# Kernel tuning notes

Hardware: AMD Instinct MI355X
Metric: run time of the kernel (lower is better)

Reference implementation:

```python
import jax, jax.numpy as jnp
import numpy as np

N_HEAD = 8
D_MODEL = 512
D_HEAD = D_MODEL // N_HEAD
D_HIDDEN = 2048
LN_EPS = 1e-5


def setup_inputs() -> dict:
    key = jax.random.key(0)
    ks = jax.random.split(key, 13)
    s = 0.02
    return {
        "spatial_features": jax.random.normal(ks[0], (4096, 64, D_MODEL), dtype=jnp.float32),
        "Wk": jax.random.normal(ks[1], (D_MODEL, D_MODEL), dtype=jnp.float32) * s,
        "bk": jnp.zeros((D_MODEL,), dtype=jnp.float32),
        "Wv": jax.random.normal(ks[2], (D_MODEL, D_MODEL), dtype=jnp.float32) * s,
        "bv": jnp.zeros((D_MODEL,), dtype=jnp.float32),
        "score_w": jax.random.normal(ks[3], (N_HEAD, D_HEAD), dtype=jnp.float32) * s,
        "score_b": jnp.zeros((N_HEAD,), dtype=jnp.float32),
        "W1": jax.random.normal(ks[4], (D_MODEL, D_HIDDEN), dtype=jnp.float32) * s,
        "b1": jnp.zeros((D_HIDDEN,), dtype=jnp.float32),
        "W2": jax.random.normal(ks[5], (D_HIDDEN, D_MODEL), dtype=jnp.float32) * s,
        "b2": jnp.zeros((D_MODEL,), dtype=jnp.float32),
        "ln_g": jnp.ones((D_MODEL,), dtype=jnp.float32),
        "ln_b": jnp.zeros((D_MODEL,), dtype=jnp.float32),
    }


def reference(spatial_features, Wk, bk, Wv, bv, score_w, score_b,
              W1, b1, W2, b2, ln_g, ln_b):
    B, N, _ = spatial_features.shape
    # k, v projections -> [B, N, H, Dh]
    k = (spatial_features @ Wk + bk).reshape(B, N, N_HEAD, D_HEAD)
    v = (spatial_features @ Wv + bv).reshape(B, N, N_HEAD, D_HEAD)
    # per-head score: Linear(d_head -> 1) batched over heads
    score = jnp.einsum('bnhd,hd->bnh', k, score_w) + score_b  # [B, N, H]
    attn = jax.nn.softmax(score, axis=1)                       # softmax over N
    # weighted sum pooling over N, then concat heads -> [B, d_model]
    feature = jnp.einsum('bnh,bnhd->bhd', attn, v).reshape(B, D_MODEL)
    # FFN with residual + layernorm (dropout = eval identity)
    h = jax.nn.gelu(feature @ W1 + b1, approximate=False)
    y = h @ W2 + b2 + feature
    mu = jnp.mean(y, axis=-1, keepdims=True)
    var = jnp.mean((y - mu) ** 2, axis=-1, keepdims=True)
    out = (y - mu) * jax.lax.rsqrt(var + LN_EPS) * ln_g + ln_b
    return out
```

## Files before the change

kernel.cpp:

```cpp
#include <hip/hip_runtime.h>
#include <hip/hip_bf16.h>

#define N_HEAD 8
#define D_MODEL 512
#define D_HEAD 64
#define D_HIDDEN 2048
#define NTOK 64
#define BATCH 4096

typedef __attribute__((ext_vector_type(4))) float f32x4;
typedef __attribute__((ext_vector_type(8))) short short8;
typedef __attribute__((ext_vector_type(8))) unsigned short u16x8;
typedef __attribute__((ext_vector_type(4))) unsigned short u16x4;

__device__ __forceinline__ float bf2f(unsigned short u) {
    return __uint_as_float(((unsigned int)u) << 16);
}
__device__ __forceinline__ unsigned short f2bf(float f) {
    unsigned int b = __float_as_uint(f);
    b += 0x7fffu + ((b >> 16) & 1u);
    return (unsigned short)(b >> 16);
}
__device__ __forceinline__ float wave_sum(float v) {
    v += __shfl_xor(v, 32); v += __shfl_xor(v, 16); v += __shfl_xor(v, 8);
    v += __shfl_xor(v, 4);  v += __shfl_xor(v, 2);  v += __shfl_xor(v, 1);
    return v;
}
__device__ __forceinline__ void gload_lds16(const void* g, void* l) {
    __builtin_amdgcn_global_load_lds(
        (const __attribute__((address_space(1))) unsigned int*)g,
        (__attribute__((address_space(3))) unsigned int*)l, 16, 0, 0);
}

__global__ __launch_bounds__(256) void prep_all(
    const float* __restrict__ Wk, const float* __restrict__ score_w,
    const float* __restrict__ Wv, const float* __restrict__ W1,
    const float* __restrict__ W2,
    unsigned short* __restrict__ uT,
    unsigned short* __restrict__ WvT, unsigned short* __restrict__ W1T,
    unsigned short* __restrict__ W2T) {
    int m = blockIdx.y;
    if (m == 3) {
        int idx = blockIdx.x * 256 + threadIdx.x;
        if (idx < 16 * 512) {
            int h = idx & 15, c = idx >> 4;
            float s = 0.f;
            if (h < 8) {
                #pragma unroll 8
                for (int d = 0; d < D_HEAD; ++d)
                    s += Wk[c * D_MODEL + h * D_HEAD + d] * score_w[h * D_HEAD + d];
            }
            uT[h * D_MODEL + c] = f2bf(s);
        }
        return;
    }
    const float* in; unsigned short* out; int K, N, tX, tiles;
    if (m == 0)      { in = Wv; out = WvT; K = 512;  N = 512;  tX = 16; tiles = 256;  }
    else if (m == 1) { in = W1; out = W1T; K = 512;  N = 2048; tX = 64; tiles = 1024; }
    else             { in = W2; out = W2T; K = 2048; N = 512;  tX = 16; tiles = 1024; }
    int t = blockIdx.x;
    if (t >= tiles) return;
    int n0 = (t % tX) * 32, k0 = (t / tX) * 32;
    __shared__ float tile[32][33];
    int tx = threadIdx.x & 31, ty = threadIdx.x >> 5;
    #pragma unroll
    for (int i = ty; i < 32; i += 8)
        tile[i][tx] = in[(size_t)(k0 + i) * N + n0 + tx];
    __syncthreads();
    #pragma unroll
    for (int i = ty; i < 32; i += 8)
        out[(size_t)(n0 + i) * K + k0 + tx] = f2bf(tile[tx][i]);
}

__global__ __launch_bounds__(256) void score_pool_v13(
    const float* __restrict__ x, const unsigned short* __restrict__ uT,
    unsigned short* __restrict__ pooled) {
    __shared__ unsigned short xl[16 * D_MODEL];
    __shared__ unsigned short ul[8 * D_MODEL];
    __shared__ float el[16 * 8];
    __shared__ float zacc[8];

    const int tid = threadIdx.x;
    const int l = tid & 63, w = tid >> 6;
    const int hg = l >> 4, lr = l & 15;

    {
        int r = tid >> 5;
        int c16 = (tid & 31) * 16;
        u16x8 v0 = *(const u16x8*)(uT + r * D_MODEL + c16);
        u16x8 v1 = *(const u16x8*)(uT + r * D_MODEL + c16 + 8);
        *(u16x8*)&ul[r * D_MODEL + ((c16) ^ (r << 3))] = v0;
        *(u16x8*)&ul[r * D_MODEL + ((c16 + 8) ^ (r << 3))] = v1;
    }

    const int trow = tid >> 7;
    const int col4 = (tid & 127) * 4;
    const int b0 = blockIdx.x * 2;

    float4 preA[8], preB[8];
    f32x4 acc[4][2];
    #pragma unroll
    for (int c = 0; c < 4; ++c) {
        acc[c][0] = (f32x4){0.f, 0.f, 0.f, 0.f};
        acc[c][1] = (f32x4){0.f, 0.f, 0.f, 0.f};
    }

    {
        const float4* p = (const float4*)(x + (size_t)b0 * (NTOK * D_MODEL));
        #pragma unroll
        for (int j = 0; j < 8; ++j) preA[j] = p[j * 256 + tid];
    }

    int qq = 0;

#define QBODY(CUR, NXT)                                                        \
    {                                                                          \
        const int q = qq & 3;                                                  \
        if (q == 0 && tid < 8) zacc[tid] = 0.f;                                \
        _Pragma("unroll")                                                      \
        for (int j = 0; j < 8; ++j) {                                          \
            int row = 2 * j + trow;                                            \
            float4 a = CUR[j];                                                 \
            u16x4 ov = {f2bf(a.x), f2bf(a.y), f2bf(a.z), f2bf(a.w)};           \
            *(u16x4*)&xl[row * D_MODEL + (col4 ^ ((row & 7) << 3))] = ov;      \
        }                                                                      \
        if (qq < 7) {                                                          \
            const int nb = b0 + ((qq + 1) >> 2), nq = (qq + 1) & 3;            \
            const float4* p = (const float4*)(x +                              \
                (size_t)nb * (NTOK * D_MODEL) + nq * 16 * D_MODEL);            \
            _Pragma("unroll")                                                  \
            for (int j = 0; j < 8; ++j) NXT[j] = p[j * 256 + tid];             \
        }                                                                      \
        asm volatile("s_waitcnt lgkmcnt(0)" ::: "memory");                     \
        __builtin_amdgcn_s_barrier();                                   \
        if (w == q) {                                                          \
            f32x4 sacc = {0.f, 0.f, 0.f, 0.f};                                 \
            const int rbase = lr * D_MODEL;                                    \
            const int rsw = (lr & 7) << 3;                                     \
            _Pragma("unroll")                                                  \
            for (int ks = 0; ks < 16; ++ks) {                                  \
                int off = ks * 32 + hg * 8;                                    \
                short8 uf;                                                     \
                if (lr < 8) uf = *(const short8*)&ul[lr * D_MODEL +            \
                                                     (off ^ (lr << 3))];       \
                else        uf = (short8){0, 0, 0, 0, 0, 0, 0, 0};             \
                short8 xf = *(const short8*)&xl[rbase + (off ^ rsw)];          \
                sacc = __builtin_amdgcn_mfma_f32_16x16x32_bf16(uf, xf, sacc,   \
                                                               0, 0, 0);       \
            }                                                                  \
            f32x4 ev;                                                          \
            float zsum[4];                                                     \
            _Pragma("unroll")                                                  \
            for (int j = 0; j < 4; ++j) {                                      \
                float e = __expf(sacc[j]);                                     \
                ev[j] = e;                                                     \
                e += __shfl_xor(e, 1); e += __shfl_xor(e, 2);                  \
                e += __shfl_xor(e, 4); e += __shfl_xor(e, 8);                  \
                zsum[j] = e;                                                   \
            }                                                                  \
            if (hg < 2) {                                                      \
                *(f32x4*)&el[lr * 8 + hg * 4] = ev;                            \
                if (lr == 0) {                                                 \
                    f32x4 z = *(const f32x4*)&zacc[hg * 4];                    \
                    z[0] += zsum[0]; z[1] += zsum[1];                          \
                    z[2] += zsum[2]; z[3] += zsum[3];                          \
                    *(f32x4*)&zacc[hg * 4] = z;                                \
                }                                                              \
            }                                                                  \
        }                                                                      \
        asm volatile("s_waitcnt lgkmcnt(0)" ::: "memory");                     \
        __builtin_amdgcn_s_barrier();                                   \
        _Pragma("unroll")                                                      \
        for (int j = 0; j < 8; ++j) {                                          \
            int t = 2 * j + trow;                                              \
            f32x4 e0 = *(const f32x4*)&el[t * 8];                              \
            f32x4 e1 = *(const f32x4*)&el[t * 8 + 4];                          \
            float4 a = CUR[j];                                                 \
            acc[0][0] += e0 * a.x; acc[0][1] += e1 * a.x;                      \
            acc[1][0] += e0 * a.y; acc[1][1] += e1 * a.y;                      \
            acc[2][0] += e0 * a.z; acc[2][1] += e1 * a.z;                      \
            acc[3][0] += e0 * a.w; acc[3][1] += e1 * a.w;                      \
        }                                                                      \
        if (q == 3) {                                                          \
            float* scr = (float*)xl;                                           \
            const int s = tid & 127;                                           \
            const int sw4 = (s & 7) << 2;                                      \
            if (trow) {                                                        \
                _Pragma("unroll")                                              \
                for (int c = 0; c < 4; ++c) {                                  \
                    _Pragma("unroll")                                          \
                    for (int hh = 0; hh < 2; ++hh)                             \
                        *(f32x4*)&scr[s * 32 +                                 \
                            (((c * 2 + hh) * 4) ^ sw4)] = acc[c][hh];          \
                }                                                              \
            }                                                                  \
            asm volatile("s_waitcnt lgkmcnt(0)" ::: "memory");                 \
            __builtin_amdgcn_s_barrier();                              \
            if (!trow) {                                                       \
                _Pragma("unroll")                                              \
                for (int c = 0; c < 4; ++c) {                                  \
                    _Pragma("unroll")                                          \
                    for (int hh = 0; hh < 2; ++hh)                             \
                        acc[c][hh] += *(const f32x4*)&scr[s * 32 +             \
                            (((c * 2 + hh) * 4) ^ sw4)];                       \
                }                                                              \
                f32x4 z0 = *(const f32x4*)&zacc[0];                            \
                f32x4 z1 = *(const f32x4*)&zacc[4];                            \
                unsigned short* pb = pooled +                                  \
                    (size_t)(b0 + (qq >> 2)) * (N_HEAD * D_MODEL);             \
                _Pragma("unroll")                                              \
                for (int h = 0; h < 8; ++h) {                                  \
                    const int hh = h >> 2, hi = h & 3;                         \
                    float rzh = 1.f / (h < 4 ? z0[hi] : z1[hi]);               \
                    u16x4 o = {f2bf(acc[0][hh][hi] * rzh),                     \
                               f2bf(acc[1][hh][hi] * rzh),                     \
                               f2bf(acc[2][hh][hi] * rzh),                     \
                               f2bf(acc[3][hh][hi] * rzh)};                    \
                    *(u16x4*)&pb[h * D_MODEL + col4] = o;                      \
                }                                                              \
            }                                                                  \
            _Pragma("unroll")                                                  \
            for (int c = 0; c < 4; ++c) {                                      \
                acc[c][0] = (f32x4){0.f, 0.f, 0.f, 0.f};                       \
                acc[c][1] = (f32x4){0.f, 0.f, 0.f, 0.f};                       \
            }                                                                  \
            asm volatile("s_waitcnt lgkmcnt(0)" ::: "memory");                 \
            __builtin_amdgcn_s_barrier();                              \
        }                                                                      \
        ++qq;                                                                  \
    }

    #pragma unroll 1
    for (int it = 0; it < 4; ++it) {
        QBODY(preA, preB)
        QBODY(preB, preA)
    }
#undef QBODY
}

template <int BM, int BN, int MODE>
__global__ __launch_bounds__(256) void gemm_mf(
    const unsigned short* __restrict__ A, int lda,
    const unsigned short* __restrict__ BT,
    const float* __restrict__ bias,
    void* __restrict__ Cout, int ldc,
    const unsigned short* __restrict__ res, int K) {
    __shared__ unsigned short Al[BM * 64];
    __shared__ unsigned short Bl[BN * 64];
    int m0 = blockIdx.x * BM;
    int n0;
    const unsigned short* Ap = A;
    const unsigned short* Bp;
    const float* bp;
    if (MODE == 0) {
        int h = blockIdx.y;
        Ap = A + (size_t)h * 512;
        Bp = BT + (size_t)h * 64 * K;
        bp = bias + h * 64;
        n0 = h * 64;
    } else {
        n0 = blockIdx.y * BN;
        Bp = BT + (size_t)n0 * K;
        bp = bias + n0;
    }
    int tid = threadIdx.x, l = tid & 63, w = tid >> 6;
    int lr = l & 15, lq = l >> 4;
    int wm = w >> 1, wn = w & 1;
    constexpr int MR = BM / 32, NR = BN / 32;
    constexpr int AI = BM / 8, BI = BN / 8;

    f32x4 acc[MR][NR];
    #pragma unroll
    for (int mi = 0; mi < MR; ++mi)
        #pragma unroll
        for (int nj = 0; nj < NR; ++nj) acc[mi][nj] = (f32x4){0.f, 0.f, 0.f, 0.f};

    int srow = l >> 3;
    int scol = ((l & 7) ^ ((l >> 3) & 7)) << 3;

    for (int k0 = 0; k0 < K; k0 += 64) {
        #pragma unroll
        for (int j = 0; j < AI / 4; ++j) {
            int ji = w * (AI / 4) + j;
            const unsigned short* src = Ap + (size_t)(m0 + ji * 8 + srow) * lda + k0 + scol;
            gload_lds16(src, &Al[ji * 512]);
        }
        #pragma unroll
        for (int j = 0; j < BI / 4; ++j) {
            int ji = w * (BI / 4) + j;
            const unsigned short* src = Bp + (size_t)(ji * 8 + srow) * K + k0 + scol;
            gload_lds16(src, &Bl[ji * 512]);
        }
        __syncthreads();
        #pragma unroll
        for (int kk = 0; kk < 64; kk += 32) {
            int sw = (kk + lq * 8) ^ ((l & 7) << 3);
            short8 af[MR], bf[NR];
            #pragma unroll
            for (int mi = 0; mi < MR; ++mi)
                af[mi] = *(const short8*)&Al[(wm * (BM / 2) + mi * 16 + lr) * 64 + sw];
            #pragma unroll
            for (int nj = 0; nj < NR; ++nj)
                bf[nj] = *(const short8*)&Bl[(wn * (BN / 2) + nj * 16 + lr) * 64 + sw];
            #pragma unroll
            for (int mi = 0; mi < MR; ++mi)
                #pragma unroll
                for (int nj = 0; nj < NR; ++nj)
                    acc[mi][nj] = __builtin_amdgcn_mfma_f32_16x16x32_bf16(
                        af[mi], bf[nj], acc[mi][nj], 0, 0, 0);
        }
        __syncthreads();
    }

    #pragma unroll
    for (int mi = 0; mi < MR; ++mi) {
        #pragma unroll
        for (int nj = 0; nj < NR; ++nj) {
            #pragma unroll
            for (int j = 0; j < 4; ++j) {
                int row = m0 + wm * (BM / 2) + mi * 16 + lq * 4 + j;
                int nl = wn * (BN / 2) + nj * 16 + lr;
                int col = n0 + nl;
                float v = acc[mi][nj][j] + bp[nl];
                if (MODE == 1) {
                    v = 0.5f * v * (1.0f + erff(v * 0.70710678118654752f));
                }
                if (MODE == 2) {
                    v += bf2f(res[(size_t)row * 512 + col]);
                    ((float*)Cout)[(size_t)row * ldc + col] = v;
                } else {
                    ((unsigned short*)Cout)[(size_t)row * ldc + col] = f2bf(v);
                }
            }
        }
    }
}

__global__ __launch_bounds__(256) void ln_kernel(
    float* __restrict__ y, const float* __restrict__ g, const float* __restrict__ bta) {
    int row = blockIdx.x * 4 + (threadIdx.x >> 6);
    int l = threadIdx.x & 63;
    float* yp = y + (size_t)row * D_MODEL;
    float4 v0 = *(const float4*)(yp + l * 8);
    float4 v1 = *(const float4*)(yp + l * 8 + 4);
    float vv[8] = {v0.x, v0.y, v0.z, v0.w, v1.x, v1.y, v1.z, v1.w};
    float s = 0.f;
    #pragma unroll
    for (int i = 0; i < 8; ++i) s += vv[i];
    s = wave_sum(s);
    float mean = s * (1.f / 512.f);
    float q = 0.f;
    #pragma unroll
    for (int i = 0; i < 8; ++i) { float d = vv[i] - mean; q += d * d; }
    q = wave_sum(q);
    float rstd = rsqrtf(q * (1.f / 512.f) + 1e-5f);
    float4 g0 = *(const float4*)(g + l * 8);
    float4 g1 = *(const float4*)(g + l * 8 + 4);
    float4 b0 = *(const float4*)(bta + l * 8);
    float4 b1 = *(const float4*)(bta + l * 8 + 4);
    float gv[8] = {g0.x, g0.y, g0.z, g0.w, g1.x, g1.y, g1.z, g1.w};
    float bv[8] = {b0.x, b0.y, b0.z, b0.w, b1.x, b1.y, b1.z, b1.w};
    float ov[8];
    #pragma unroll
    for (int i = 0; i < 8; ++i) ov[i] = (vv[i] - mean) * rstd * gv[i] + bv[i];
    float4 o0 = {ov[0], ov[1], ov[2], ov[3]};
    float4 o1 = {ov[4], ov[5], ov[6], ov[7]};
    *(float4*)(yp + l * 8) = o0;
    *(float4*)(yp + l * 8 + 4) = o1;
}

extern "C" void kernel_launch(void* const* d_in, const int* in_sizes, int n_in,
                              void* d_out, int out_size, void* d_ws, size_t ws_size,
                              hipStream_t stream) {
    const float* x       = (const float*)d_in[0];
    const float* Wk      = (const float*)d_in[1];
    const float* Wv      = (const float*)d_in[3];
    const float* bv      = (const float*)d_in[4];
    const float* score_w = (const float*)d_in[5];
    const float* W1      = (const float*)d_in[7];
    const float* b1      = (const float*)d_in[8];
    const float* W2      = (const float*)d_in[9];
    const float* b2      = (const float*)d_in[10];
    const float* ln_g    = (const float*)d_in[11];
    const float* ln_b    = (const float*)d_in[12];
    float* out = (float*)d_out;

    char* ws = (char*)d_ws;
    size_t off = 0;
    auto alloc = [&](size_t sz) {
        void* p = ws + off;
        off = (off + sz + 1023) & ~(size_t)1023;
        return p;
    };
    unsigned short* uT  = (unsigned short*)alloc((size_t)16 * D_MODEL * 2);
    unsigned short* WvT = (unsigned short*)alloc((size_t)512 * 512 * 2);
    unsigned short* W1T = (unsigned short*)alloc((size_t)2048 * 512 * 2);
    unsigned short* W2T = (unsigned short*)alloc((size_t)512 * 2048 * 2);
    unsigned short* pooled = (unsigned short*)alloc((size_t)BATCH * N_HEAD * D_MODEL * 2);
    unsigned short* feat   = (unsigned short*)alloc((size_t)BATCH * D_MODEL * 2);
    unsigned short* Hbuf   = (unsigned short*)alloc((size_t)BATCH * D_HIDDEN * 2);

    prep_all<<<dim3(1024, 4), dim3(256), 0, stream>>>(
        Wk, score_w, Wv, W1, W2, uT, WvT, W1T, W2T);
    score_pool_v13<<<dim3(2048), dim3(256), 0, stream>>>(x, uT, pooled);
    gemm_mf<128, 64, 0><<<dim3(32, 8), dim3(256), 0, stream>>>(
        pooled, N_HEAD * D_MODEL, WvT, bv, (void*)feat, D_MODEL,
        (const unsigned short*)nullptr, 512);
    gemm_mf<128, 128, 1><<<dim3(32, 16), dim3(256), 0, stream>>>(
        feat, D_MODEL, W1T, b1, (void*)Hbuf, D_HIDDEN,
        (const unsigned short*)nullptr, 512);
    gemm_mf<64, 128, 2><<<dim3(64, 4), dim3(256), 0, stream>>>(
        Hbuf, D_HIDDEN, W2T, b2, (void*)out, D_MODEL, feat, 2048);
    ln_kernel<<<dim3(1024), dim3(256), 0, stream>>>(out, ln_g, ln_b);
}
```

Baseline: 236.2 us.

## Restructure score-pool kernel to 512 threads with bf16 LDS pooling

The score/pool kernel now runs 512-thread blocks covering four batches each, with half as many blocks. Each thread owns two columns and one half of the heads, so the cross-thread reduction through scratch LDS and its extra barriers go away. Pooling now reads the bf16 tile from LDS instead of keeping fp32 registers, and the prefetch runs two quarters ahead using two buffers. The trade-offs are bf16-rounded x in the weighted sum, more LDS reads, an extra barrier every step, and no launch_bounds on a 512-thread kernel, which could affect register allocation.

After: 209.9 us. 11.1% less time.

```diff
diff --git a/kernel.cpp b/kernel.cpp
--- a/kernel.cpp
+++ b/kernel.cpp
@@ -72,7 +72,7 @@
         out[(size_t)(n0 + i) * K + k0 + tx] = f2bf(tile[tx][i]);
 }
 
-__global__ __launch_bounds__(256) void score_pool_v13(
+__global__ void score_pool_v15(
     const float* __restrict__ x, const unsigned short* __restrict__ uT,
     unsigned short* __restrict__ pooled) {
     __shared__ unsigned short xl[16 * D_MODEL];
@@ -85,55 +85,57 @@
     const int hg = l >> 4, lr = l & 15;
 
     {
-        int r = tid >> 5;
-        int c16 = (tid & 31) * 16;
-        u16x8 v0 = *(const u16x8*)(uT + r * D_MODEL + c16);
-        u16x8 v1 = *(const u16x8*)(uT + r * D_MODEL + c16 + 8);
-        *(u16x8*)&ul[r * D_MODEL + ((c16) ^ (r << 3))] = v0;
-        *(u16x8*)&ul[r * D_MODEL + ((c16 + 8) ^ (r << 3))] = v1;
-    }
-
-    const int trow = tid >> 7;
+        int r = tid >> 6;
+        int c8 = (tid & 63) * 8;
+        u16x8 v = *(const u16x8*)(uT + r * D_MODEL + c8);
+        *(u16x8*)&ul[r * D_MODEL + (c8 ^ (r << 3))] = v;
+    }
+
+    const int tr4 = tid >> 7;
     const int col4 = (tid & 127) * 4;
-    const int b0 = blockIdx.x * 2;
-
-    float4 preA[8], preB[8];
-    f32x4 acc[4][2];
-    #pragma unroll
-    for (int c = 0; c < 4; ++c) {
-        acc[c][0] = (f32x4){0.f, 0.f, 0.f, 0.f};
-        acc[c][1] = (f32x4){0.f, 0.f, 0.f, 0.f};
-    }
-
+
+    const int c2 = (tid & 255) * 2;
+    const int hh = tid >> 8;
+
+    const int b0 = blockIdx.x * 4;
+
+    float4 preA[4], preB[4];
     {
-        const float4* p = (const float4*)(x + (size_t)b0 * (NTOK * D_MODEL));
-        #pragma unroll
-        for (int j = 0; j < 8; ++j) preA[j] = p[j * 256 + tid];
-    }
+        const float4* p0 = (const float4*)(x + (size_t)b0 * (NTOK * D_MODEL));
+        const float4* p1 = (const float4*)(x + (size_t)b0 * (NTOK * D_MODEL) +
+                                           16 * D_MODEL);
+        #pragma unroll
+        for (int j = 0; j < 4; ++j) preA[j] = p0[j * 512 + tid];
+        #pragma unroll
+        for (int j = 0; j < 4; ++j) preB[j] = p1[j * 512 + tid];
+    }
+
+    f32x4 acc0 = {0.f, 0.f, 0.f, 0.f};
+    f32x4 acc1 = {0.f, 0.f, 0.f, 0.f};
 
     int qq = 0;
 
-#define QBODY(CUR, NXT)                                                        \
+#define QSTEP(BUF)                                                             \
     {                                                                          \
         const int q = qq & 3;                                                  \
         if (q == 0 && tid < 8) zacc[tid] = 0.f;                                \
         _Pragma("unroll")                                                      \
-        for (int j = 0; j < 8; ++j) {                                          \
-            int row = 2 * j + trow;                                            \
-            float4 a = CUR[j];                                                 \
+        for (int j = 0; j < 4; ++j) {                                          \
+            int row = j * 4 + tr4;                                             \
+            float4 a = BUF[j];                                                 \
             u16x4 ov = {f2bf(a.x), f2bf(a.y), f2bf(a.z), f2bf(a.w)};           \
             *(u16x4*)&xl[row * D_MODEL + (col4 ^ ((row & 7) << 3))] = ov;      \
         }                                                                      \
-        if (qq < 7) {                                                          \
-            const int nb = b0 + ((qq + 1) >> 2), nq = (qq + 1) & 3;            \
+        if (qq < 14) {                                                         \
+            const int nb = b0 + ((qq + 2) >> 2), nq = (qq + 2) & 3;            \
             const float4* p = (const float4*)(x +                              \
                 (size_t)nb * (NTOK * D_MODEL) + nq * 16 * D_MODEL);            \
             _Pragma("unroll")                                                  \
-            for (int j = 0; j < 8; ++j) NXT[j] = p[j * 256 + tid];             \
+            for (int j = 0; j < 4; ++j) BUF[j] = p[j * 512 + tid];             \
         }                                                                      \
         asm volatile("s_waitcnt lgkmcnt(0)" ::: "memory");                     \
         __builtin_amdgcn_s_barrier();                                   \
-        if (w == q) {                                                          \
+        if (w == (qq & 7)) {                                                   \
             f32x4 sacc = {0.f, 0.f, 0.f, 0.f};                                 \
             const int rbase = lr * D_MODEL;                                    \
             const int rsw = (lr & 7) << 3;                                     \
@@ -170,72 +172,41 @@
         }                                                                      \
         asm volatile("s_waitcnt lgkmcnt(0)" ::: "memory");                     \
         __builtin_amdgcn_s_barrier();                                   \
-        _Pragma("unroll")                                                      \
-        for (int j = 0; j < 8; ++j) {                                          \
-            int t = 2 * j + trow;                                              \
-            f32x4 e0 = *(const f32x4*)&el[t * 8];                              \
-            f32x4 e1 = *(const f32x4*)&el[t * 8 + 4];                          \
-            float4 a = CUR[j];                                                 \
-            acc[0][0] += e0 * a.x; acc[0][1] += e1 * a.x;                      \
-            acc[1][0] += e0 * a.y; acc[1][1] += e1 * a.y;                      \
-            acc[2][0] += e0 * a.z; acc[2][1] += e1 * a.z;                      \
-            acc[3][0] += e0 * a.w; acc[3][1] += e1 * a.w;                      \
+        _Pragma("unroll 4")                                                    \
+        for (int t = 0; t < 16; ++t) {                                         \
+            unsigned int xw = *(const unsigned int*)&xl[t * D_MODEL +          \
+                                                  (c2 ^ ((t & 7) << 3))];      \
+            f32x4 e4 = *(const f32x4*)&el[t * 8 + hh * 4];                     \
+            float xa = __uint_as_float(xw << 16);                              \
+            float xb = __uint_as_float(xw & 0xffff0000u);                      \
+            acc0 += e4 * xa;                                                   \
+            acc1 += e4 * xb;                                                   \
         }                                                                      \
         if (q == 3) {                                                          \
-            float* scr = (float*)xl;                                           \
-            const int s = tid & 127;                                           \
-            const int sw4 = (s & 7) << 2;                                      \
-            if (trow) {                                                        \
-                _Pragma("unroll")                                              \
-                for (int c = 0; c < 4; ++c) {                                  \
-                    _Pragma("unroll")                                          \
-                    for (int hh = 0; hh < 2; ++hh)                             \
-                        *(f32x4*)&scr[s * 32 +                                 \
-                            (((c * 2 + hh) * 4) ^ sw4)] = acc[c][hh];          \
-                }                                                              \
+            f32x4 z = *(const f32x4*)&zacc[hh * 4];                            \
+            unsigned short* pb = pooled +                                      \
+                (size_t)(b0 + (qq >> 2)) * (N_HEAD * D_MODEL);                 \
+            _Pragma("unroll")                                                  \
+            for (int hq = 0; hq < 4; ++hq) {                                   \
+                float rzq = 1.f / z[hq];                                       \
+                unsigned int pk = (unsigned int)f2bf(acc0[hq] * rzq) |         \
+                                  ((unsigned int)f2bf(acc1[hq] * rzq) << 16);  \
+                *(unsigned int*)(pb + (hh * 4 + hq) * D_MODEL + c2) = pk;      \
             }                                                                  \
-            asm volatile("s_waitcnt lgkmcnt(0)" ::: "memory");                 \
-            __builtin_amdgcn_s_barrier();                              \
-            if (!trow) {                                                       \
-                _Pragma("unroll")                                              \
-                for (int c = 0; c < 4; ++c) {                                  \
-                    _Pragma("unroll")                                          \
-                    for (int hh = 0; hh < 2; ++hh)                             \
-                        acc[c][hh] += *(const f32x4*)&scr[s * 32 +             \
-                            (((c * 2 + hh) * 4) ^ sw4)];                       \
-                }                                                              \
-                f32x4 z0 = *(const f32x4*)&zacc[0];                            \
-                f32x4 z1 = *(const f32x4*)&zacc[4];                            \
-                unsigned short* pb = pooled +                                  \
-                    (size_t)(b0 + (qq >> 2)) * (N_HEAD * D_MODEL);             \
-                _Pragma("unroll")                                              \
-                for (int h = 0; h < 8; ++h) {                                  \
-                    const int hh = h >> 2, hi = h & 3;                         \
-                    float rzh = 1.f / (h < 4 ? z0[hi] : z1[hi]);               \
-                    u16x4 o = {f2bf(acc[0][hh][hi] * rzh),                     \
-                               f2bf(acc[1][hh][hi] * rzh),                     \
-                               f2bf(acc[2][hh][hi] * rzh),                     \
-                               f2bf(acc[3][hh][hi] * rzh)};                    \
-                    *(u16x4*)&pb[h * D_MODEL + col4] = o;                      \
-                }                                                              \
-            }                                                                  \
-            _Pragma("unroll")                                                  \
-            for (int c = 0; c < 4; ++c) {                                      \
-                acc[c][0] = (f32x4){0.f, 0.f, 0.f, 0.f};                       \
-                acc[c][1] = (f32x4){0.f, 0.f, 0.f, 0.f};                       \
-            }                                                                  \
-            asm volatile("s_waitcnt lgkmcnt(0)" ::: "memory");                 \
-            __builtin_amdgcn_s_barrier();                              \
-        }                                                                      \
+            acc0 = (f32x4){0.f, 0.f, 0.f, 0.f};                                \
+            acc1 = (f32x4){0.f, 0.f, 0.f, 0.f};                                \
+        }                                                                      \
+        asm volatile("s_waitcnt lgkmcnt(0)" ::: "memory");                     \
+        __builtin_amdgcn_s_barrier();                                   \
         ++qq;                                                                  \
     }
 
     #pragma unroll 1
-    for (int it = 0; it < 4; ++it) {
-        QBODY(preA, preB)
-        QBODY(preB, preA)
-    }
-#undef QBODY
+    for (int it = 0; it < 8; ++it) {
+        QSTEP(preA)
+        QSTEP(preB)
+    }
+#undef QSTEP
 }
 
 template <int BM, int BN, int MODE>
@@ -402,7 +373,7 @@
 
     prep_all<<<dim3(1024, 4), dim3(256), 0, stream>>>(
         Wk, score_w, Wv, W1, W2, uT, WvT, W1T, W2T);
-    score_pool_v13<<<dim3(2048), dim3(256), 0, stream>>>(x, uT, pooled);
+    score_pool_v15<<<dim3(1024), dim3(512), 0, stream>>>(x, uT, pooled);
     gemm_mf<128, 64, 0><<<dim3(32, 8), dim3(256), 0, stream>>>(
         pooled, N_HEAD * D_MODEL, WvT, bv, (void*)feat, D_MODEL,
         (const unsigned short*)nullptr, 512);
```
